# Kernel tuning notes

Hardware: AMD Instinct MI355X
Metric: run time of the kernel (lower is better)

## Reference

```python
import jax, jax.numpy as jnp
from jax import lax
import numpy as np

H = 64  # hiddenSize
I = 9   # inputSize

def _init_lstm_params(key, in_dim, hidden):
    k = 1.0 / np.sqrt(hidden)
    ks = jax.random.split(key, 4)
    w_ih = jax.random.uniform(ks[0], (4 * hidden, in_dim), minval=-k, maxval=k, dtype=jnp.float32)
    w_hh = jax.random.uniform(ks[1], (4 * hidden, hidden), minval=-k, maxval=k, dtype=jnp.float32)
    b_ih = jax.random.uniform(ks[2], (4 * hidden,), minval=-k, maxval=k, dtype=jnp.float32)
    b_hh = jax.random.uniform(ks[3], (4 * hidden,), minval=-k, maxval=k, dtype=jnp.float32)
    return w_ih, w_hh, b_ih, b_hh

def setup_inputs() -> dict:
    key = jax.random.key(0)
    kx, k0, k1, kl = jax.random.split(key, 4)
    x = jax.random.normal(kx, (4096, 336, I), dtype=jnp.float32)
    w_ih0, w_hh0, b_ih0, b_hh0 = _init_lstm_params(k0, I, H)
    w_ih1, w_hh1, b_ih1, b_hh1 = _init_lstm_params(k1, H, H)
    klw, klb = jax.random.split(kl)
    k = 1.0 / np.sqrt(H)
    w_lin = jax.random.uniform(klw, (1, H), minval=-k, maxval=k, dtype=jnp.float32)
    b_lin = jax.random.uniform(klb, (1,), minval=-k, maxval=k, dtype=jnp.float32)
    return {"x": x, "w_ih0": w_ih0, "w_hh0": w_hh0, "b_ih0": b_ih0, "b_hh0": b_hh0,
            "w_ih1": w_ih1, "w_hh1": w_hh1, "b_ih1": b_ih1, "b_hh1": b_hh1,
            "w_lin": w_lin, "b_lin": b_lin}

def _lstm_layer(x_seq, w_ih, w_hh, b_ih, b_hh):
    # x_seq: [B, T, D] -> hidden sequence [B, T, H]. PyTorch gate order: i, f, g, o.
    B = x_seq.shape[0]
    hidden = w_hh.shape[1]
    # Precompute input contribution for all timesteps in one GEMM.
    pre = jnp.einsum('btd,gd->btg', x_seq, w_ih) + b_ih + b_hh  # [B, T, 4H]
    pre_t = jnp.swapaxes(pre, 0, 1)  # [T, B, 4H]

    def step(carry, p):
        h, c = carry
        gates = p + h @ w_hh.T  # [B, 4H]
        i, f, g, o = jnp.split(gates, 4, axis=-1)
        i = jax.nn.sigmoid(i)
        f = jax.nn.sigmoid(f)
        g = jnp.tanh(g)
        o = jax.nn.sigmoid(o)
        c = f * c + i * g
        h = o * jnp.tanh(c)
        return (h, c), h

    h0 = jnp.zeros((B, hidden), dtype=x_seq.dtype)
    c0 = jnp.zeros((B, hidden), dtype=x_seq.dtype)
    _, hs = lax.scan(step, (h0, c0), pre_t)
    return jnp.swapaxes(hs, 0, 1)  # [B, T, H]

def reference(x, w_ih0, w_hh0, b_ih0, b_hh0, w_ih1, w_hh1, b_ih1, b_hh1, w_lin, b_lin):
    h1 = _lstm_layer(x, w_ih0, w_hh0, b_ih0, b_hh0)     # layer 1 (dropout inactive in eval)
    h2 = _lstm_layer(h1, w_ih1, w_hh1, b_ih1, b_hh1)    # layer 2
    last = h2[:, -1, :]                                  # [B, H]
    out = jax.nn.sigmoid(last @ w_lin.T + b_lin)         # [B, 1]
    return out
```

## Files before the change

### kernel.cpp

```cpp
#include <hip/hip_runtime.h>
#include <hip/hip_bf16.h>
#include <stdint.h>


typedef __attribute__((ext_vector_type(8))) short s16x8;
typedef __attribute__((ext_vector_type(4))) short s16x4;
typedef __attribute__((ext_vector_type(4))) float f32x4;

#define MFMA_BF16 __builtin_amdgcn_mfma_f32_16x16x32_bf16
#define LOG2E     1.4426950408889634f
#define TWO_LOG2E 2.8853900817779268f

__device__ __forceinline__ short f2bf(float f) {
    uint32_t u = __builtin_bit_cast(uint32_t, f);
    u += 0x7fffu + ((u >> 16) & 1u);
    return (short)(u >> 16);
}

__device__ __forceinline__ s16x4 pack_bf16x4(float a, float b, float c, float d) {
    union { uint32_t u[2]; s16x4 s; } r;
    asm("v_cvt_pk_bf16_f32 %0, %1, %2" : "=v"(r.u[0]) : "v"(a), "v"(b));
    asm("v_cvt_pk_bf16_f32 %0, %1, %2" : "=v"(r.u[1]) : "v"(c), "v"(d));
    return r.s;
}

static __device__ __forceinline__ float fexp2(float t){ return __builtin_amdgcn_exp2f(t); }
static __device__ __forceinline__ float frcp (float t){ return __builtin_amdgcn_rcpf(t); }

__device__ __forceinline__ float rcp1p2(float t) {
    return frcp(1.0f + fexp2(t));
}

__device__ __forceinline__ f32x4 nonlin_wide(const f32x4 acc[4], f32x4& c) {
    float e0[4], e1[4], e2[4], e3[4];
    #pragma unroll
    for (int r = 0; r < 4; ++r) {
        e0[r] = fexp2(acc[0][r]);
        e1[r] = fexp2(acc[1][r]);
        e2[r] = fexp2(acc[2][r]);
        e3[r] = fexp2(acc[3][r]);
    }
    float iv[4], fv[4], gq[4], ov[4];
    #pragma unroll
    for (int r = 0; r < 4; ++r) {
        iv[r] = frcp(1.f + e0[r]);
        fv[r] = frcp(1.f + e1[r]);
        gq[r] = frcp(1.f + e2[r]);
        ov[r] = frcp(1.f + e3[r]);
    }
    float ec[4];
    #pragma unroll
    for (int r = 0; r < 4; ++r) {
        float gv = fmaf(-2.f, gq[r], 1.f);
        c[r] = fmaf(fv[r], c[r], iv[r] * gv);
        ec[r] = fexp2(c[r] * TWO_LOG2E);
    }
    f32x4 h;
    #pragma unroll
    for (int r = 0; r < 4; ++r) {
        float th = fmaf(-2.f, frcp(1.f + ec[r]), 1.f);
        h[r] = ov[r] * th;
    }
    return h;
}

__global__ __launch_bounds__(512, 1)
void lstm_fused(const float* __restrict__ x,
                const float* __restrict__ w_ih0, const float* __restrict__ w_hh0,
                const float* __restrict__ b_ih0, const float* __restrict__ b_hh0,
                const float* __restrict__ w_ih1, const float* __restrict__ w_hh1,
                const float* __restrict__ b_ih1, const float* __restrict__ b_hh1,
                const float* __restrict__ w_lin, const float* __restrict__ b_lin,
                float* __restrict__ out)
{
    __shared__ __align__(16) short xs[16 * 512];
    __shared__ __align__(16) short h0s[2][16 * 64];
    __shared__ __align__(16) short h1s[16 * 64];
    __shared__ float red[4][16];

    const int tid  = threadIdx.x;
    const int w    = tid >> 6;
    const int role = w >> 2;
    const int wl   = w & 3;
    const int l    = tid & 63;
    const int bcol = l & 15;
    const int q    = l >> 4;
    const int b0   = blockIdx.x * 16;

    for (int i = tid; i < 16 * 512; i += 512) xs[i] = 0;
    for (int i = tid; i < 16 * 64; i += 512) {
        h0s[0][i] = 0; h0s[1][i] = 0; h1s[i] = 0;
    }
    __syncthreads();

    const float scm[4] = { -LOG2E, -LOG2E, TWO_LOG2E, -LOG2E };

    s16x8 aW[4][4];
    f32x4 bias[4];
    #pragma unroll
    for (int m = 0; m < 4; ++m) {
        const int R = m * 64 + wl * 16 + bcol;
        const float sc = scm[m];
        if (role == 0) {
            #pragma unroll
            for (int r = 0; r < 8; ++r) {
                int k = q * 8 + r;
                aW[m][0][r] = (k < 9) ? f2bf(w_ih0[R * 9 + k] * sc) : (short)0;
            }
            #pragma unroll
            for (int kf = 0; kf < 2; ++kf) {
                const float* p = w_hh0 + R * 64 + kf * 32 + q * 8;
                #pragma unroll
                for (int r = 0; r < 8; ++r) aW[m][1 + kf][r] = f2bf(p[r] * sc);
            }
            #pragma unroll
            for (int r = 0; r < 8; ++r) aW[m][3][r] = 0;
            #pragma unroll
            for (int r = 0; r < 4; ++r) {
                int G = m * 64 + wl * 16 + q * 4 + r;
                bias[m][r] = (b_ih0[G] + b_hh0[G]) * sc;
            }
        } else {
            #pragma unroll
            for (int kf = 0; kf < 4; ++kf) {
                int ks = kf * 32 + q * 8;
                const float* p = (ks < 64) ? (w_ih1 + R * 64 + ks)
                                           : (w_hh1 + R * 64 + (ks - 64));
                #pragma unroll
                for (int r = 0; r < 8; ++r) aW[m][kf][r] = f2bf(p[r] * sc);
            }
            #pragma unroll
            for (int r = 0; r < 4; ++r) {
                int G = m * 64 + wl * 16 + q * 4 + r;
                bias[m][r] = (b_ih1[G] + b_hh1[G]) * sc;
            }
        }
    }

    f32x4 c  = {0.f, 0.f, 0.f, 0.f};
    f32x4 hq = {0.f, 0.f, 0.f, 0.f};
    f32x4 accL1[4];
    #pragma unroll
    for (int m = 0; m < 4; ++m) accL1[m] = (f32x4){0.f, 0.f, 0.f, 0.f};

    const int hrd0 = bcol * 64 + (((q    ) ^ (bcol & 7)) << 3);
    const int hrd1 = bcol * 64 + (((4 + q) ^ (bcol & 7)) << 3);
    const int hwr  = bcol * 64 + (((wl * 2 + (q >> 1)) ^ (bcol & 7)) << 3)
                   + ((q & 1) << 2);
    const int xrd  = bcol * 32 + ((q ^ (bcol & 3)) << 3);

    const int    ld_b = (tid & 255) >> 4, ld_t = tid & 15;
    const float* xrow = x + (size_t)(b0 + ld_b) * (336 * 9) + ld_t * 9;
    const int    xs_wr_base = ld_t * 512 + ld_b * 32;
    const int    xswzw = (ld_b & 3) << 3;

    #pragma unroll 1
    for (int i = 0; i <= 337; ++i) {
        if ((i & 15) == 0 && i < 336) {
            if (tid < 256) {
                const float* xp = xrow + (size_t)i * 9;
                #pragma unroll
                for (int d = 0; d < 9; ++d)
                    xs[(xs_wr_base + d) ^ xswzw] = f2bf(xp[d]);
            }
            __syncthreads();
        }

        f32x4 acc0[4];
        if (role == 0) {
            if (i <= 335) {
                s16x8 bx = *(const s16x8*)&xs[(i & 15) * 512 + xrd];
                const short* h0r = h0s[(i & 1) ^ 1];
                s16x8 ba = *(const s16x8*)&h0r[hrd0];
                s16x8 bb = *(const s16x8*)&h0r[hrd1];
                #pragma unroll
                for (int m = 0; m < 4; ++m) acc0[m] = MFMA_BF16(aW[m][0], bx, bias[m], 0, 0, 0);
                #pragma unroll
                for (int m = 0; m < 4; ++m) acc0[m] = MFMA_BF16(aW[m][1], ba, acc0[m], 0, 0, 0);
                #pragma unroll
                for (int m = 0; m < 4; ++m) acc0[m] = MFMA_BF16(aW[m][2], bb, acc0[m], 0, 0, 0);
            }
        } else {
            if (i >= 2) {
                __builtin_amdgcn_s_setprio(1);
                hq = nonlin_wide(accL1, c);
                __builtin_amdgcn_s_setprio(0);
                *(s16x4*)&h1s[hwr] = pack_bf16x4(hq[0], hq[1], hq[2], hq[3]);
            }
        }
        __syncthreads();

        if (role == 0) {
            if (i <= 335) {
                __builtin_amdgcn_s_setprio(1);
                hq = nonlin_wide(acc0, c);
                __builtin_amdgcn_s_setprio(0);
                short* h0w = h0s[i & 1];
                *(s16x4*)&h0w[hwr] = pack_bf16x4(hq[0], hq[1], hq[2], hq[3]);
            }
        } else {
            if (i >= 1 && i <= 336) {
                const short* h0r = h0s[(i & 1) ^ 1];
                s16x8 ba  = *(const s16x8*)&h0r[hrd0];
                s16x8 bb  = *(const s16x8*)&h0r[hrd1];
                s16x8 b1a = *(const s16x8*)&h1s[hrd0];
                s16x8 b1b = *(const s16x8*)&h1s[hrd1];
                #pragma unroll
                for (int m = 0; m < 4; ++m) accL1[m] = MFMA_BF16(aW[m][0], ba,  bias[m], 0, 0, 0);
                #pragma unroll
                for (int m = 0; m < 4; ++m) accL1[m] = MFMA_BF16(aW[m][1], bb,  accL1[m], 0, 0, 0);
                #pragma unroll
                for (int m = 0; m < 4; ++m) accL1[m] = MFMA_BF16(aW[m][2], b1a, accL1[m], 0, 0, 0);
                #pragma unroll
                for (int m = 0; m < 4; ++m) accL1[m] = MFMA_BF16(aW[m][3], b1b, accL1[m], 0, 0, 0);
            }
        }
        __syncthreads();
    }

    if (role == 1) {
        float part = hq[0] * w_lin[wl * 16 + q * 4 + 0]
                   + hq[1] * w_lin[wl * 16 + q * 4 + 1]
                   + hq[2] * w_lin[wl * 16 + q * 4 + 2]
                   + hq[3] * w_lin[wl * 16 + q * 4 + 3];
        part += __shfl_xor(part, 16, 64);
        part += __shfl_xor(part, 32, 64);
        if (q == 0) red[wl][bcol] = part;
    }
    __syncthreads();
    if (tid < 16) {
        float s = red[0][tid] + red[1][tid] + red[2][tid] + red[3][tid] + b_lin[0];
        out[b0 + tid] = rcp1p2(-s * LOG2E);
    }
}

extern "C" void kernel_launch(void* const* d_in, const int* in_sizes, int n_in,
                              void* d_out, int out_size, void* d_ws, size_t ws_size,
                              hipStream_t stream) {
    const float* x     = (const float*)d_in[0];
    const float* w_ih0 = (const float*)d_in[1];
    const float* w_hh0 = (const float*)d_in[2];
    const float* b_ih0 = (const float*)d_in[3];
    const float* b_hh0 = (const float*)d_in[4];
    const float* w_ih1 = (const float*)d_in[5];
    const float* w_hh1 = (const float*)d_in[6];
    const float* b_ih1 = (const float*)d_in[7];
    const float* b_hh1 = (const float*)d_in[8];
    const float* w_lin = (const float*)d_in[9];
    const float* b_lin = (const float*)d_in[10];

    lstm_fused<<<dim3(256), dim3(512), 0, stream>>>(
        x, w_ih0, w_hh0, b_ih0, b_hh0,
        w_ih1, w_hh1, b_ih1, b_hh1,
        w_lin, b_lin, (float*)d_out);
}
```

Before: 293.2 us.

## Share reciprocals across LSTM gates, prefetch x chunks, hoist layer-1 h0 loads

The gate nonlinearity now computes one reciprocal for the product of four sigmoid denominators and recovers each gate by multiplication. The tanh(c) step likewise shares one reciprocal between pairs. Exponent inputs are clamped with fmed3 so the products cannot overflow. The next 16-step x chunk is loaded into registers right after the barrier, hiding global load latency. Layer-1 warps read their h0 operands before the first barrier, overlapping the LDS reads with the nonlinearity. The cost is extra multiplies and clamps in exchange for fewer transcendental rcp ops on the serial critical path, plus a small accuracy change from the shared reciprocal and clamping.

```diff
diff --git a/kernel.cpp b/kernel.cpp
--- a/kernel.cpp
+++ b/kernel.cpp
@@ -26,41 +26,51 @@
 
 static __device__ __forceinline__ float fexp2(float t){ return __builtin_amdgcn_exp2f(t); }
 static __device__ __forceinline__ float frcp (float t){ return __builtin_amdgcn_rcpf(t); }
+static __device__ __forceinline__ float fclmp(float v, float lo, float hi){
+    return __builtin_amdgcn_fmed3f(v, lo, hi);
+}
 
 __device__ __forceinline__ float rcp1p2(float t) {
     return frcp(1.0f + fexp2(t));
 }
 
-__device__ __forceinline__ f32x4 nonlin_wide(const f32x4 acc[4], f32x4& c) {
+__device__ __forceinline__ f32x4 nonlin_qw(const f32x4 acc[4], f32x4& c) {
     float e0[4], e1[4], e2[4], e3[4];
     #pragma unroll
     for (int r = 0; r < 4; ++r) {
-        e0[r] = fexp2(acc[0][r]);
-        e1[r] = fexp2(acc[1][r]);
-        e2[r] = fexp2(acc[2][r]);
-        e3[r] = fexp2(acc[3][r]);
-    }
-    float iv[4], fv[4], gq[4], ov[4];
+        e0[r] = fexp2(fclmp(acc[0][r], -30.f, 30.f));
+        e1[r] = fexp2(fclmp(acc[1][r], -30.f, 30.f));
+        e2[r] = fexp2(fclmp(acc[2][r], -30.f, 30.f));
+        e3[r] = fexp2(fclmp(acc[3][r], -30.f, 30.f));
+    }
+    float d0[4], d1[4], d2[4], d3[4], p01[4], p23[4], rr[4];
     #pragma unroll
     for (int r = 0; r < 4; ++r) {
-        iv[r] = frcp(1.f + e0[r]);
-        fv[r] = frcp(1.f + e1[r]);
-        gq[r] = frcp(1.f + e2[r]);
-        ov[r] = frcp(1.f + e3[r]);
-    }
-    float ec[4];
+        d0[r] = 1.f + e0[r]; d1[r] = 1.f + e1[r];
+        d2[r] = 1.f + e2[r]; d3[r] = 1.f + e3[r];
+        p01[r] = d0[r] * d1[r]; p23[r] = d2[r] * d3[r];
+    }
+    #pragma unroll
+    for (int r = 0; r < 4; ++r) rr[r] = frcp(p01[r] * p23[r]);
+    float ov[4], ec[4];
     #pragma unroll
     for (int r = 0; r < 4; ++r) {
-        float gv = fmaf(-2.f, gq[r], 1.f);
-        c[r] = fmaf(fv[r], c[r], iv[r] * gv);
-        ec[r] = fexp2(c[r] * TWO_LOG2E);
+        float q01 = rr[r] * p23[r], q23 = rr[r] * p01[r];
+        float iv = q01 * d1[r], fv = q01 * d0[r];
+        float gv = fmaf(-2.f, q23 * d3[r], 1.f);
+        ov[r] = q23 * d2[r];
+        c[r] = fmaf(fv, c[r], iv * gv);
+        ec[r] = fexp2(fclmp(c[r] * TWO_LOG2E, -28.f, 28.f));
     }
     f32x4 h;
-    #pragma unroll
-    for (int r = 0; r < 4; ++r) {
-        float th = fmaf(-2.f, frcp(1.f + ec[r]), 1.f);
-        h[r] = ov[r] * th;
-    }
+    {   float dg0 = 1.f + ec[0], dg1 = 1.f + ec[1];
+        float rg = frcp(dg0 * dg1);
+        h[0] = ov[0] * fmaf(-2.f, rg * dg1, 1.f);
+        h[1] = ov[1] * fmaf(-2.f, rg * dg0, 1.f); }
+    {   float dg2 = 1.f + ec[2], dg3 = 1.f + ec[3];
+        float rg = frcp(dg2 * dg3);
+        h[2] = ov[2] * fmaf(-2.f, rg * dg3, 1.f);
+        h[3] = ov[3] * fmaf(-2.f, rg * dg2, 1.f); }
     return h;
 }
 
@@ -154,19 +164,30 @@
     const int    xs_wr_base = ld_t * 512 + ld_b * 32;
     const int    xswzw = (ld_b & 3) << 3;
 
+    float xreg[9];
+    if (tid < 256) {
+        #pragma unroll
+        for (int d = 0; d < 9; ++d) xreg[d] = xrow[d];
+    }
+
     #pragma unroll 1
     for (int i = 0; i <= 337; ++i) {
         if ((i & 15) == 0 && i < 336) {
             if (tid < 256) {
-                const float* xp = xrow + (size_t)i * 9;
                 #pragma unroll
                 for (int d = 0; d < 9; ++d)
-                    xs[(xs_wr_base + d) ^ xswzw] = f2bf(xp[d]);
+                    xs[(xs_wr_base + d) ^ xswzw] = f2bf(xreg[d]);
             }
             __syncthreads();
+            if (tid < 256 && i + 16 < 336) {
+                const float* xp = xrow + (size_t)(i + 16) * 9;
+                #pragma unroll
+                for (int d = 0; d < 9; ++d) xreg[d] = xp[d];
+            }
         }
 
         f32x4 acc0[4];
+        s16x8 ba1, bb1;
         if (role == 0) {
             if (i <= 335) {
                 s16x8 bx = *(const s16x8*)&xs[(i & 15) * 512 + xrd];
@@ -181,9 +202,14 @@
                 for (int m = 0; m < 4; ++m) acc0[m] = MFMA_BF16(aW[m][2], bb, acc0[m], 0, 0, 0);
             }
         } else {
+            if (i >= 1 && i <= 336) {
+                const short* h0r = h0s[(i & 1) ^ 1];
+                ba1 = *(const s16x8*)&h0r[hrd0];
+                bb1 = *(const s16x8*)&h0r[hrd1];
+            }
             if (i >= 2) {
                 __builtin_amdgcn_s_setprio(1);
-                hq = nonlin_wide(accL1, c);
+                hq = nonlin_qw(accL1, c);
                 __builtin_amdgcn_s_setprio(0);
                 *(s16x4*)&h1s[hwr] = pack_bf16x4(hq[0], hq[1], hq[2], hq[3]);
             }
@@ -193,22 +219,19 @@
         if (role == 0) {
             if (i <= 335) {
                 __builtin_amdgcn_s_setprio(1);
-                hq = nonlin_wide(acc0, c);
+                hq = nonlin_qw(acc0, c);
                 __builtin_amdgcn_s_setprio(0);
                 short* h0w = h0s[i & 1];
                 *(s16x4*)&h0w[hwr] = pack_bf16x4(hq[0], hq[1], hq[2], hq[3]);
             }
         } else {
             if (i >= 1 && i <= 336) {
-                const short* h0r = h0s[(i & 1) ^ 1];
-                s16x8 ba  = *(const s16x8*)&h0r[hrd0];
-                s16x8 bb  = *(const s16x8*)&h0r[hrd1];
                 s16x8 b1a = *(const s16x8*)&h1s[hrd0];
                 s16x8 b1b = *(const s16x8*)&h1s[hrd1];
                 #pragma unroll
-                for (int m = 0; m < 4; ++m) accL1[m] = MFMA_BF16(aW[m][0], ba,  bias[m], 0, 0, 0);
-                #pragma unroll
-                for (int m = 0; m < 4; ++m) accL1[m] = MFMA_BF16(aW[m][1], bb,  accL1[m], 0, 0, 0);
+                for (int m = 0; m < 4; ++m) accL1[m] = MFMA_BF16(aW[m][0], ba1, bias[m], 0, 0, 0);
+                #pragma unroll
+                for (int m = 0; m < 4; ++m) accL1[m] = MFMA_BF16(aW[m][1], bb1, accL1[m], 0, 0, 0);
                 #pragma unroll
                 for (int m = 0; m < 4; ++m) accL1[m] = MFMA_BF16(aW[m][2], b1a, accL1[m], 0, 0, 0);
                 #pragma unroll
```

Result: slower. 312.9 us (+6.7%).
